# Performance work log

Hardware: AMD Instinct MI355X
Metric: run time of the kernel (lower is better)

## Reference

```python
import jax, jax.numpy as jnp
import numpy as np

B, D, H, S = 65536, 256, 4, 64
HD = D // H  # head_dim = 64
EPS = 1e-8


def _lin(x, W, b):
    # torch nn.Linear: y = x @ W.T + b, W: [out, in]
    return x @ W.T + b


def _cos_attn(q_heads, keys, vals):
    # q_heads: [B,H,hd]; keys/vals: [H,S,hd] (shared across batch)
    qn = q_heads / (jnp.linalg.norm(q_heads, axis=-1, keepdims=True) + EPS)
    kn = keys / (jnp.linalg.norm(keys, axis=-1, keepdims=True) + EPS)
    sim = jnp.einsum('bhd,hsd->bhs', qn, kn)          # cosine sims, temp=1.0
    attn = jax.nn.softmax(sim, axis=-1)
    return jnp.einsum('bhs,hsd->bhd', attn, vals)     # [B,H,hd]


def setup_inputs() -> dict:
    key = jax.random.key(0)
    ks = jax.random.split(key, 20)

    def xavier(k, shape):
        fan_in, fan_out = shape[1], shape[0]
        lim = np.sqrt(6.0 / (fan_in + fan_out))
        return jax.random.uniform(k, shape, jnp.float32, -lim, lim)

    return {
        'query': jax.random.normal(ks[0], (B, D), jnp.float32),
        'context': jax.random.normal(ks[1], (B, D), jnp.float32),
        'fast_keys': 0.01 * jax.random.normal(ks[2], (H, S, HD), jnp.float32),
        'fast_vals': 0.01 * jax.random.normal(ks[3], (H, S, HD), jnp.float32),
        'deep_keys': 0.01 * jax.random.normal(ks[4], (H, S, HD), jnp.float32),
        'deep_vals': 0.01 * jax.random.normal(ks[5], (H, S, HD), jnp.float32),
        'Wq': xavier(ks[6], (D, D)), 'bq': jnp.zeros((D,), jnp.float32),
        'Wg': xavier(ks[7], (D, D)), 'bg': jnp.zeros((D,), jnp.float32),
        'Wc1': xavier(ks[8], (D // 2, D)), 'bc1': jnp.zeros((D // 2,), jnp.float32),
        'Wc2': xavier(ks[9], (1, D // 2)), 'bc2': jnp.zeros((1,), jnp.float32),
        'Wo': xavier(ks[10], (D, D)), 'bo': jnp.zeros((D,), jnp.float32),
        'Ws': xavier(ks[11], (D, D)), 'bs': jnp.zeros((D,), jnp.float32),
        'mix_logit': jnp.zeros((), jnp.float32),
        'surprise_mean': jnp.zeros((1, D), jnp.float32),
        'surprise_var': jnp.ones((1, D), jnp.float32),
    }


def reference(query, context, fast_keys, fast_vals, deep_keys, deep_vals,
              Wq, bq, Wg, bg, Wc1, bc1, Wc2, bc2, Wo, bo, Ws, bs,
              mix_logit, surprise_mean, surprise_var):
    # --- query projection and head split ---
    q = _lin(query, Wq, bq)                       # [B, D]
    q_heads = q.reshape(B, H, HD)                 # [B, H, hd]

    # --- dual-tier cosine-similarity attention reads ---
    v_fast = _cos_attn(q_heads, fast_keys, fast_vals).reshape(B, D)
    v_deep = _cos_attn(q_heads, deep_keys, deep_vals).reshape(B, D)

    # --- context-gated mixing of tiers ---
    gate = jnp.tanh(_lin(context, Wg, bg)).mean(axis=-1, keepdims=True)  # [B,1]
    mix = jax.nn.sigmoid(mix_logit + gate)
    out = mix * v_fast + (1.0 - mix) * v_deep

    # --- adaptive retrieval confidence head ---
    conf = jax.nn.sigmoid(_lin(jnp.tanh(_lin(context, Wc1, bc1)), Wc2, bc2))  # [B,1]
    out = out * conf
    out = _lin(out, Wo, bo)                       # [B, d_value]

    # --- surprise (detached diagnostic, does not feed output) ---
    h = jax.lax.stop_gradient(_lin(context, Ws, bs))
    z = (h - surprise_mean) / jnp.sqrt(surprise_var + 1e-6)
    surprise = jax.nn.sigmoid(jnp.abs(z).mean(axis=-1) - 2.0)  # 1/max(0.5,0.1)=2.0
    del surprise  # aux diagnostic; main output is the retrieved vector
    return out
```

## Files before the change

kernel.cpp:

```cpp
#include <hip/hip_runtime.h>

typedef unsigned short u16;
typedef __attribute__((ext_vector_type(8))) short bf16x8;
typedef __attribute__((ext_vector_type(4))) float f32x4;
typedef __attribute__((ext_vector_type(8))) unsigned short u16x8;

#define MFMA16(a, b, c) __builtin_amdgcn_mfma_f32_16x16x32_bf16((a), (b), (c), 0, 0, 0)

#define OFF_WQ   0
#define OFF_WG   65536
#define OFF_WC1  131072
#define OFF_WO   163840
#define OFF_KNF  229376
#define OFF_VTF  245760
#define OFF_KND  262144
#define OFF_VTD  278528

__device__ __forceinline__ u16 f2b(float f) {
  union { float f; unsigned u; } v; v.f = f;
  unsigned r = v.u + 0x7fffu + ((v.u >> 16) & 1u);
  return (u16)(r >> 16);
}
__device__ __forceinline__ unsigned pk2(float lo, float hi) {
  unsigned r;
  asm("v_cvt_pk_bf16_f32 %0, %1, %2" : "=v"(r) : "v"(lo), "v"(hi));
  return r;
}
__device__ __forceinline__ float fsig(float x) {
  return __builtin_amdgcn_rcpf(1.f + __expf(-x));
}
__device__ __forceinline__ float ftanh(float x) {
  float e = __expf(2.f * x);
  return (e - 1.f) * __builtin_amdgcn_rcpf(e + 1.f);
}
__device__ __forceinline__ float sum16(float v) {
  v += __shfl_xor(v, 1);
  v += __shfl_xor(v, 2);
  v += __shfl_xor(v, 4);
  v += __shfl_xor(v, 8);
  return v;
}

__global__ void k_prep(const float* __restrict__ Wq, const float* __restrict__ Wg,
                       const float* __restrict__ Wc1, const float* __restrict__ Wo,
                       const float* __restrict__ fk, const float* __restrict__ fv,
                       const float* __restrict__ dk, const float* __restrict__ dv,
                       u16* __restrict__ ws) {
  const int bid = blockIdx.x, t = threadIdx.x;
  if (bid < 96) {
    const float* W = bid < 32 ? Wq : (bid < 64 ? Wg : Wo);
    const int OFF = bid < 32 ? OFF_WQ : (bid < 64 ? OFF_WG : OFF_WO);
    int c = (bid & 31) * 256 + t;
    int lane = c & 63, nt = (c >> 6) & 1, kk = (c >> 7) & 7, w = c >> 10;
    const float* s = W + (w * 32 + nt * 16 + (lane & 15)) * 256 + kk * 32 + ((lane >> 4) & 3) * 8;
    u16x8 o;
    #pragma unroll
    for (int j = 0; j < 8; ++j) o[j] = f2b(s[j]);
    *(u16x8*)(ws + OFF + c * 8) = o;
  } else if (bid < 112) {
    int c = (bid - 96) * 256 + t;
    int lane = c & 63, kk = (c >> 6) & 7, w = c >> 9;
    const float* s = Wc1 + (w * 16 + (lane & 15)) * 256 + kk * 32 + ((lane >> 4) & 3) * 8;
    u16x8 o;
    #pragma unroll
    for (int j = 0; j < 8; ++j) o[j] = f2b(s[j]);
    *(u16x8*)(ws + OFF_WC1 + c * 8) = o;
  } else {
    int unit = (bid - 112) * 4 + (t >> 6);
    int lane = t & 63;
    int st = unit >> 8, rowid = unit & 255;
    int hh = rowid >> 6, s = rowid & 63;
    if (st < 2) {
      const float* p = (st == 0 ? fk : dk) + rowid * 64;
      float x = p[lane];
      float v = x * x;
      v += __shfl_xor(v, 1);  v += __shfl_xor(v, 2);  v += __shfl_xor(v, 4);
      v += __shfl_xor(v, 8);  v += __shfl_xor(v, 16); v += __shfl_xor(v, 32);
      float sc = __builtin_amdgcn_rcpf(__builtin_amdgcn_sqrtf(v) + 1e-8f);
      int nt = s >> 4, kk = lane >> 5, lo = ((lane >> 3) & 3) * 16 + (s & 15), j = lane & 7;
      ws[(st == 0 ? OFF_KNF : OFF_KND) + (((hh * 2 + kk) * 4 + nt) * 64 + lo) * 8 + j] =
          f2b(x * sc);
    } else {
      const float* p = (st == 2 ? fv : dv) + rowid * 64;
      int kk = s >> 5, qd = (s >> 3) & 3, j = s & 7;
      int lo = qd * 16 + (lane & 15), nt = lane >> 4;
      ws[(st == 2 ? OFF_VTF : OFF_VTD) + (((hh * 2 + kk) * 4 + nt) * 64 + lo) * 8 + j] =
          f2b(p[lane]);
    }
  }
}

__global__ __launch_bounds__(512, 4)
void k_fused(const float* __restrict__ query, const float* __restrict__ context,
             const float* __restrict__ bq, const float* __restrict__ bg,
             const float* __restrict__ bc1, const float* __restrict__ Wc2,
             const float* __restrict__ bc2v, const float* __restrict__ bo,
             const float* __restrict__ mixl, const u16* __restrict__ ws,
             float* __restrict__ outp) {
  __shared__ u16 sX[64 * 256];
  __shared__ u16 sY[64 * 256];
  __shared__ float red_a[8][64];
  __shared__ float red_c[8][64];
  __shared__ float sA[64];
  __shared__ float sB[64];

  const int t = threadIdx.x;
  const int w = t >> 6;
  const int lane = t & 63;
  const int quad = lane >> 4;
  const int l16 = lane & 15;
  const int row4 = quad * 4;
  const int l16e = l16 & ~1;
  const int oddl = lane & 1;
  const int hd = w & 3;
  const int rb = (w >> 2) * 32;
  const int blk = blockIdx.x;
  char* Xb = (char*)sX;
  char* Yb = (char*)sY;
  char* Ch = Xb + w * 4096;

  auto stage = [&](char* dstB, const float* src) {
    #pragma unroll
    for (int i = 0; i < 8; ++i) {
      int e = i * 2048 + t * 4;
      float4 v = *(const float4*)(src + e);
      int row = e >> 8, col = e & 255;
      uint2 pk;
      pk.x = pk2(v.x, v.y);
      pk.y = pk2(v.z, v.w);
      *(uint2*)(dstB + row * 512 + ((((col >> 3) ^ (row & 7)) << 4) | ((col & 7) << 1))) = pk;
    }
  };
  auto ldA = [&](const char* B, int row, int kb) {
    return *(const bf16x8*)(B + row * 512 + ((((kb >> 3) ^ (row & 7)) << 4)));
  };
  auto ldCh = [&](int row, int kb) {
    return *(const bf16x8*)(Ch + row * 128 + ((((kb >> 3) ^ (row & 7)) << 4)));
  };
  auto st4c = [&](int row, float v0, float v1, float v2, float v3) {
    float o0 = __shfl_xor(v0, 1), o1 = __shfl_xor(v1, 1);
    float o2 = __shfl_xor(v2, 1), o3 = __shfl_xor(v3, 1);
    float lo0 = oddl ? o1 : v0, hi0 = oddl ? v1 : o0;
    float lo1 = oddl ? o3 : v2, hi1 = oddl ? v3 : o2;
    int c0 = (oddl ? 16 : 0) + l16e, c1 = (oddl ? 48 : 32) + l16e;
    *(unsigned*)(Ch + row * 128 + ((((c0 >> 3) ^ (row & 7)) << 4) | ((c0 & 7) << 1))) = pk2(lo0, hi0);
    *(unsigned*)(Ch + row * 128 + ((((c1 >> 3) ^ (row & 7)) << 4) | ((c1 & 7) << 1))) = pk2(lo1, hi1);
  };
  auto st4y = [&](int row, int cb, float v0, float v1, float v2, float v3) {
    float o0 = __shfl_xor(v0, 1), o1 = __shfl_xor(v1, 1);
    float o2 = __shfl_xor(v2, 1), o3 = __shfl_xor(v3, 1);
    float lo0 = oddl ? o1 : v0, hi0 = oddl ? v1 : o0;
    float lo1 = oddl ? o3 : v2, hi1 = oddl ? v3 : o2;
    int c0 = cb + (oddl ? 16 : 0) + l16e, c1 = cb + (oddl ? 48 : 32) + l16e;
    *(unsigned*)(Yb + row * 512 + ((((c0 >> 3) ^ (row & 7)) << 4) | ((c0 & 7) << 1))) = pk2(lo0, hi0);
    *(unsigned*)(Yb + row * 512 + ((((c1 >> 3) ^ (row & 7)) << 4) | ((c1 & 7) << 1))) = pk2(lo1, hi1);
  };

  const f32x4 vzero = {0.f, 0.f, 0.f, 0.f};

  bf16x8 pg0 = *(const bf16x8*)(ws + OFF_WG + ((w * 16 + 0) * 64 + lane) * 8);
  bf16x8 pg1 = *(const bf16x8*)(ws + OFF_WG + ((w * 16 + 1) * 64 + lane) * 8);
  bf16x8 pc0 = *(const bf16x8*)(ws + OFF_WC1 + ((w * 8) * 64 + lane) * 8);

  stage(Xb, context + (size_t)blk * 16384);
  stage(Yb, query + (size_t)blk * 16384);
  float bgv[2], bov[2], bq4[4];
  #pragma unroll
  for (int nt = 0; nt < 2; ++nt) {
    int n = w * 32 + nt * 16 + l16;
    bgv[nt] = bg[n]; bov[nt] = bo[n];
  }
  #pragma unroll
  for (int nt = 0; nt < 4; ++nt) bq4[nt] = bq[hd * 64 + nt * 16 + l16];
  float bc1v = bc1[w * 16 + l16];
  float wc2v = Wc2[w * 16 + l16];
  __syncthreads();

  bf16x8 pq0, pq1;
  {
    f32x4 ag[4][2], ac[4];
    #pragma unroll
    for (int mt = 0; mt < 4; ++mt) { ag[mt][0] = vzero; ag[mt][1] = vzero; ac[mt] = vzero; }
    #pragma unroll
    for (int kk = 0; kk < 8; ++kk) {
      int kb = kk * 32 + quad * 8;
      bf16x8 a0 = ldA(Xb, l16, kb), a1 = ldA(Xb, 16 + l16, kb),
             a2 = ldA(Xb, 32 + l16, kb), a3 = ldA(Xb, 48 + l16, kb);
      bf16x8 b0 = kk ? *(const bf16x8*)(ws + OFF_WG + (((w * 8 + kk) * 2 + 0) * 64 + lane) * 8) : pg0;
      bf16x8 b1 = kk ? *(const bf16x8*)(ws + OFF_WG + (((w * 8 + kk) * 2 + 1) * 64 + lane) * 8) : pg1;
      bf16x8 bc = kk ? *(const bf16x8*)(ws + OFF_WC1 + ((w * 8 + kk) * 64 + lane) * 8) : pc0;
      ag[0][0] = MFMA16(a0, b0, ag[0][0]); ag[0][1] = MFMA16(a0, b1, ag[0][1]);
      ag[1][0] = MFMA16(a1, b0, ag[1][0]); ag[1][1] = MFMA16(a1, b1, ag[1][1]);
      ag[2][0] = MFMA16(a2, b0, ag[2][0]); ag[2][1] = MFMA16(a2, b1, ag[2][1]);
      ag[3][0] = MFMA16(a3, b0, ag[3][0]); ag[3][1] = MFMA16(a3, b1, ag[3][1]);
      ac[0] = MFMA16(a0, bc, ac[0]);
      ac[1] = MFMA16(a1, bc, ac[1]);
      ac[2] = MFMA16(a2, bc, ac[2]);
      ac[3] = MFMA16(a3, bc, ac[3]);
    }
    pq0 = *(const bf16x8*)(ws + OFF_WQ + ((((hd * 4) >> 1) * 8 * 2 + ((hd * 4) & 1)) * 64 + lane) * 8);
    pq1 = *(const bf16x8*)(ws + OFF_WQ + (((((hd * 4 + 1) >> 1) * 8) * 2 + ((hd * 4 + 1) & 1)) * 64 + lane) * 8);
    #pragma unroll
    for (int mt = 0; mt < 4; ++mt)
      #pragma unroll
      for (int r = 0; r < 4; ++r) {
        float sg = ftanh(ag[mt][0][r] + bgv[0]) + ftanh(ag[mt][1][r] + bgv[1]);
        sg = sum16(sg);
        float sc = ftanh(ac[mt][r] + bc1v) * wc2v;
        sc = sum16(sc);
        if (l16 == 0) { red_a[w][mt * 16 + row4 + r] = sg; red_c[w][mt * 16 + row4 + r] = sc; }
      }
  }
  __syncthreads();

  if (t < 64) {
    float g = 0.f, cc = 0.f;
    #pragma unroll
    for (int i = 0; i < 8; ++i) { g += red_a[i][t]; cc += red_c[i][t]; }
    float mix = fsig(mixl[0] + g * (1.f / 256.f));
    float conf = fsig(cc + bc2v[0]);
    sA[t] = conf * mix;
    sB[t] = conf - conf * mix;
  }
  {
    f32x4 qa[2][4];
    #pragma unroll
    for (int mt = 0; mt < 2; ++mt)
      #pragma unroll
      for (int nt = 0; nt < 4; ++nt) qa[mt][nt] = vzero;
    #pragma unroll
    for (int kk = 0; kk < 8; ++kk) {
      int kb = kk * 32 + quad * 8;
      bf16x8 a0 = ldA(Yb, rb + l16, kb), a1 = ldA(Yb, rb + 16 + l16, kb);
      #pragma unroll
      for (int nt = 0; nt < 4; ++nt) {
        int g = hd * 4 + nt;
        bf16x8 b = (kk == 0 && nt == 0) ? pq0
                 : (kk == 0 && nt == 1) ? pq1
                 : *(const bf16x8*)(ws + OFF_WQ + ((((g >> 1) * 8 + kk) * 2 + (g & 1)) * 64 + lane) * 8);
        qa[0][nt] = MFMA16(a0, b, qa[0][nt]);
        qa[1][nt] = MFMA16(a1, b, qa[1][nt]);
      }
    }
    #pragma unroll
    for (int mt = 0; mt < 2; ++mt)
      #pragma unroll
      for (int r = 0; r < 4; ++r) {
        float ss = 0.f;
        #pragma unroll
        for (int nt = 0; nt < 4; ++nt) {
          float q_ = qa[mt][nt][r] + bq4[nt];
          qa[mt][nt][r] = q_;
          ss += q_ * q_;
        }
        ss = sum16(ss);
        float scl = __builtin_amdgcn_rcpf(__builtin_amdgcn_sqrtf(ss) + 1e-8f);
        st4c(mt * 16 + row4 + r,
             qa[mt][0][r] * scl, qa[mt][1][r] * scl, qa[mt][2][r] * scl, qa[mt][3][r] * scl);
      }
  }
  __syncthreads();

  #pragma unroll
  for (int half = 0; half < 2; ++half) {
    const int rl = half * 16;
    bf16x8 q0 = ldCh(rl + l16, quad * 8);
    bf16x8 q1 = ldCh(rl + l16, 32 + quad * 8);
    f32x4 oa[4];

    #pragma unroll
    for (int tier = 0; tier < 2; ++tier) {
      const u16* KN = ws + (tier == 0 ? OFF_KNF : OFF_KND);
      const u16* VT = ws + (tier == 0 ? OFF_VTF : OFF_VTD);

      f32x4 s4[4];
      #pragma unroll
      for (int nt = 0; nt < 4; ++nt) s4[nt] = vzero;
      #pragma unroll
      for (int kk = 0; kk < 2; ++kk)
        #pragma unroll
        for (int nt = 0; nt < 4; ++nt) {
          bf16x8 b = *(const bf16x8*)(KN + (((hd * 2 + kk) * 4 + nt) * 64 + lane) * 8);
          s4[nt] = MFMA16(kk ? q1 : q0, b, s4[nt]);
        }

      #pragma unroll
      for (int r = 0; r < 4; ++r) {
        float rs = 0.f;
        #pragma unroll
        for (int nt = 0; nt < 4; ++nt) { float e = __expf(s4[nt][r]); s4[nt][r] = e; rs += e; }
        rs = sum16(rs);
        float inv = __builtin_amdgcn_rcpf(rs);
        st4c(rl + row4 + r,
             s4[0][r] * inv, s4[1][r] * inv, s4[2][r] * inv, s4[3][r] * inv);
      }

      bf16x8 p0 = ldCh(rl + l16, quad * 8);
      bf16x8 p1 = ldCh(rl + l16, 32 + quad * 8);
      f32x4 pv4[4];
      #pragma unroll
      for (int nt = 0; nt < 4; ++nt) pv4[nt] = vzero;
      #pragma unroll
      for (int kk = 0; kk < 2; ++kk)
        #pragma unroll
        for (int nt = 0; nt < 4; ++nt) {
          bf16x8 b = *(const bf16x8*)(VT + (((hd * 2 + kk) * 4 + nt) * 64 + lane) * 8);
          pv4[nt] = MFMA16(kk ? p1 : p0, b, pv4[nt]);
        }

      #pragma unroll
      for (int r = 0; r < 4; ++r) {
        int rg = rb + rl + row4 + r;
        float m_ = (tier == 0) ? sA[rg] : sB[rg];
        #pragma unroll
        for (int nt = 0; nt < 4; ++nt) {
          if (tier == 0) oa[nt][r] = m_ * pv4[nt][r];
          else           oa[nt][r] += m_ * pv4[nt][r];
        }
      }
    }

    #pragma unroll
    for (int r = 0; r < 4; ++r)
      st4y(rb + rl + row4 + r, hd * 64, oa[0][r], oa[1][r], oa[2][r], oa[3][r]);
  }

  bf16x8 po0 = *(const bf16x8*)(ws + OFF_WO + (((w * 8) * 2 + 0) * 64 + lane) * 8);
  bf16x8 po1 = *(const bf16x8*)(ws + OFF_WO + (((w * 8) * 2 + 1) * 64 + lane) * 8);
  __syncthreads();

  {
    f32x4 o[4][2];
    #pragma unroll
    for (int mt = 0; mt < 4; ++mt) { o[mt][0] = vzero; o[mt][1] = vzero; }
    #pragma unroll
    for (int kk = 0; kk < 8; ++kk) {
      int kb = kk * 32 + quad * 8;
      bf16x8 a0 = ldA(Yb, l16, kb), a1 = ldA(Yb, 16 + l16, kb),
             a2 = ldA(Yb, 32 + l16, kb), a3 = ldA(Yb, 48 + l16, kb);
      #pragma unroll
      for (int nt = 0; nt < 2; ++nt) {
        bf16x8 b = (kk == 0 && nt == 0) ? po0
                 : (kk == 0 && nt == 1) ? po1
                 : *(const bf16x8*)(ws + OFF_WO + (((w * 8 + kk) * 2 + nt) * 64 + lane) * 8);
        o[0][nt] = MFMA16(a0, b, o[0][nt]);
        o[1][nt] = MFMA16(a1, b, o[1][nt]);
        o[2][nt] = MFMA16(a2, b, o[2][nt]);
        o[3][nt] = MFMA16(a3, b, o[3][nt]);
      }
    }
    float* dst = outp + (size_t)blk * 16384;
    #pragma unroll
    for (int mt = 0; mt < 4; ++mt)
      #pragma unroll
      for (int r = 0; r < 4; ++r) {
        int row = mt * 16 + row4 + r;
        #pragma unroll
        for (int nt = 0; nt < 2; ++nt)
          dst[row * 256 + w * 32 + nt * 16 + l16] = o[mt][nt][r] + bov[nt];
      }
  }
}

extern "C" void kernel_launch(void* const* d_in, const int* in_sizes, int n_in,
                              void* d_out, int out_size, void* d_ws, size_t ws_size,
                              hipStream_t stream) {
  const float* query   = (const float*)d_in[0];
  const float* context = (const float*)d_in[1];
  const float* fk      = (const float*)d_in[2];
  const float* fv      = (const float*)d_in[3];
  const float* dk      = (const float*)d_in[4];
  const float* dv      = (const float*)d_in[5];
  const float* Wq      = (const float*)d_in[6];
  const float* bq      = (const float*)d_in[7];
  const float* Wg      = (const float*)d_in[8];
  const float* bg      = (const float*)d_in[9];
  const float* Wc1     = (const float*)d_in[10];
  const float* bc1     = (const float*)d_in[11];
  const float* Wc2     = (const float*)d_in[12];
  const float* bc2     = (const float*)d_in[13];
  const float* Wo      = (const float*)d_in[14];
  const float* bo      = (const float*)d_in[15];
  const float* mixl    = (const float*)d_in[18];
  u16* ws = (u16*)d_ws;
  float* outp = (float*)d_out;

  k_prep<<<368, 256, 0, stream>>>(Wq, Wg, Wc1, Wo, fk, fv, dk, dv, ws);
  k_fused<<<1024, 512, 0, stream>>>(query, context, bq, bg, bc1, Wc2, bc2, bo,
                                    mixl, ws, outp);
}
```

Before: 276.3 us.

## Double block to 128 rows with 16 waves and dynamic shared memory

The fused kernel now processes 128 rows per block with 1024 threads (16 waves) instead of 64 rows with 512 threads. Each wave owns one 16-column weight fragment and sweeps all 8 row tiles, so each weight fragment is fetched once per 128 rows. Q-norm reduction now crosses waves through shared memory. It uses about 149 KB of dynamic LDS, limiting each CU to one block, which trades occupancy and latency hiding for weight reuse and fewer blocks.

```diff
diff --git a/kernel.cpp b/kernel.cpp
--- a/kernel.cpp
+++ b/kernel.cpp
@@ -90,19 +90,21 @@
   }
 }
 
-__global__ __launch_bounds__(512, 4)
+__global__ __launch_bounds__(1024, 4)
 void k_fused(const float* __restrict__ query, const float* __restrict__ context,
              const float* __restrict__ bq, const float* __restrict__ bg,
              const float* __restrict__ bc1, const float* __restrict__ Wc2,
              const float* __restrict__ bc2v, const float* __restrict__ bo,
              const float* __restrict__ mixl, const u16* __restrict__ ws,
              float* __restrict__ outp) {
-  __shared__ u16 sX[64 * 256];
-  __shared__ u16 sY[64 * 256];
-  __shared__ float red_a[8][64];
-  __shared__ float red_c[8][64];
-  __shared__ float sA[64];
-  __shared__ float sB[64];
+  extern __shared__ char smem[];
+  char* Xb = smem;
+  char* Yb = smem + 65536;
+  float* red_a = (float*)(smem + 131072);
+  float* red_c = (float*)(smem + 139264);
+  float* red_q = (float*)(smem + 143360);
+  float* sA    = (float*)(smem + 151552);
+  float* sB    = (float*)(smem + 152064);
 
   const int t = threadIdx.x;
   const int w = t >> 6;
@@ -114,15 +116,15 @@
   const int oddl = lane & 1;
   const int hd = w & 3;
   const int rb = (w >> 2) * 32;
+  const int hdc = w >> 2;
+  const int cg = w & 3;
   const int blk = blockIdx.x;
-  char* Xb = (char*)sX;
-  char* Yb = (char*)sY;
   char* Ch = Xb + w * 4096;
 
   auto stage = [&](char* dstB, const float* src) {
     #pragma unroll
     for (int i = 0; i < 8; ++i) {
-      int e = i * 2048 + t * 4;
+      int e = i * 4096 + t * 4;
       float4 v = *(const float4*)(src + e);
       int row = e >> 8, col = e & 255;
       uint2 pk;
@@ -136,6 +138,9 @@
   };
   auto ldCh = [&](int row, int kb) {
     return *(const bf16x8*)(Ch + row * 128 + ((((kb >> 3) ^ (row & 7)) << 4)));
+  };
+  auto wfrag = [&](int OFF, int g, int kk) {
+    return *(const bf16x8*)(ws + OFF + ((((g >> 1) * 8 + kk) * 2 + (g & 1)) * 64 + lane) * 8);
   };
   auto st4c = [&](int row, float v0, float v1, float v2, float v3) {
     float o0 = __shfl_xor(v0, 1), o1 = __shfl_xor(v1, 1);
@@ -158,207 +163,221 @@
 
   const f32x4 vzero = {0.f, 0.f, 0.f, 0.f};
 
-  bf16x8 pg0 = *(const bf16x8*)(ws + OFF_WG + ((w * 16 + 0) * 64 + lane) * 8);
-  bf16x8 pg1 = *(const bf16x8*)(ws + OFF_WG + ((w * 16 + 1) * 64 + lane) * 8);
-  bf16x8 pc0 = *(const bf16x8*)(ws + OFF_WC1 + ((w * 8) * 64 + lane) * 8);
-
-  stage(Xb, context + (size_t)blk * 16384);
-  stage(Yb, query + (size_t)blk * 16384);
-  float bgv[2], bov[2], bq4[4];
-  #pragma unroll
-  for (int nt = 0; nt < 2; ++nt) {
-    int n = w * 32 + nt * 16 + l16;
-    bgv[nt] = bg[n]; bov[nt] = bo[n];
-  }
-  #pragma unroll
-  for (int nt = 0; nt < 4; ++nt) bq4[nt] = bq[hd * 64 + nt * 16 + l16];
-  float bc1v = bc1[w * 16 + l16];
-  float wc2v = Wc2[w * 16 + l16];
+  stage(Xb, context + (size_t)blk * 32768);
+  stage(Yb, query + (size_t)blk * 32768);
+  float bgv  = bg[w * 16 + l16];
+  float bov  = bo[w * 16 + l16];
+  float bqv  = bq[w * 16 + l16];
+  float bc1v = bc1[(w & 7) * 16 + l16];
+  float wc2v = Wc2[(w & 7) * 16 + l16];
   __syncthreads();
 
-  bf16x8 pq0, pq1;
   {
-    f32x4 ag[4][2], ac[4];
-    #pragma unroll
-    for (int mt = 0; mt < 4; ++mt) { ag[mt][0] = vzero; ag[mt][1] = vzero; ac[mt] = vzero; }
+    f32x4 ag[8];
+    #pragma unroll
+    for (int mt = 0; mt < 8; ++mt) ag[mt] = vzero;
     #pragma unroll
     for (int kk = 0; kk < 8; ++kk) {
       int kb = kk * 32 + quad * 8;
-      bf16x8 a0 = ldA(Xb, l16, kb), a1 = ldA(Xb, 16 + l16, kb),
-             a2 = ldA(Xb, 32 + l16, kb), a3 = ldA(Xb, 48 + l16, kb);
-      bf16x8 b0 = kk ? *(const bf16x8*)(ws + OFF_WG + (((w * 8 + kk) * 2 + 0) * 64 + lane) * 8) : pg0;
-      bf16x8 b1 = kk ? *(const bf16x8*)(ws + OFF_WG + (((w * 8 + kk) * 2 + 1) * 64 + lane) * 8) : pg1;
-      bf16x8 bc = kk ? *(const bf16x8*)(ws + OFF_WC1 + ((w * 8 + kk) * 64 + lane) * 8) : pc0;
-      ag[0][0] = MFMA16(a0, b0, ag[0][0]); ag[0][1] = MFMA16(a0, b1, ag[0][1]);
-      ag[1][0] = MFMA16(a1, b0, ag[1][0]); ag[1][1] = MFMA16(a1, b1, ag[1][1]);
-      ag[2][0] = MFMA16(a2, b0, ag[2][0]); ag[2][1] = MFMA16(a2, b1, ag[2][1]);
-      ag[3][0] = MFMA16(a3, b0, ag[3][0]); ag[3][1] = MFMA16(a3, b1, ag[3][1]);
-      ac[0] = MFMA16(a0, bc, ac[0]);
-      ac[1] = MFMA16(a1, bc, ac[1]);
-      ac[2] = MFMA16(a2, bc, ac[2]);
-      ac[3] = MFMA16(a3, bc, ac[3]);
-    }
-    pq0 = *(const bf16x8*)(ws + OFF_WQ + ((((hd * 4) >> 1) * 8 * 2 + ((hd * 4) & 1)) * 64 + lane) * 8);
-    pq1 = *(const bf16x8*)(ws + OFF_WQ + (((((hd * 4 + 1) >> 1) * 8) * 2 + ((hd * 4 + 1) & 1)) * 64 + lane) * 8);
-    #pragma unroll
-    for (int mt = 0; mt < 4; ++mt)
+      bf16x8 b = wfrag(OFF_WG, w, kk);
+      #pragma unroll
+      for (int mt = 0; mt < 8; ++mt) {
+        bf16x8 a = ldA(Xb, mt * 16 + l16, kb);
+        ag[mt] = MFMA16(a, b, ag[mt]);
+      }
+    }
+    #pragma unroll
+    for (int mt = 0; mt < 8; ++mt)
       #pragma unroll
       for (int r = 0; r < 4; ++r) {
-        float sg = ftanh(ag[mt][0][r] + bgv[0]) + ftanh(ag[mt][1][r] + bgv[1]);
-        sg = sum16(sg);
-        float sc = ftanh(ac[mt][r] + bc1v) * wc2v;
-        sc = sum16(sc);
-        if (l16 == 0) { red_a[w][mt * 16 + row4 + r] = sg; red_c[w][mt * 16 + row4 + r] = sc; }
+        float sg = sum16(ftanh(ag[mt][r] + bgv));
+        if (l16 == 0) red_a[(mt * 16 + row4 + r) * 16 + w] = sg;
+      }
+  }
+  {
+    const int mtb = (w < 8) ? 0 : 4;
+    f32x4 ac[4];
+    #pragma unroll
+    for (int m = 0; m < 4; ++m) ac[m] = vzero;
+    #pragma unroll
+    for (int kk = 0; kk < 8; ++kk) {
+      int kb = kk * 32 + quad * 8;
+      bf16x8 b = *(const bf16x8*)(ws + OFF_WC1 + (((w & 7) * 8 + kk) * 64 + lane) * 8);
+      #pragma unroll
+      for (int m = 0; m < 4; ++m) {
+        bf16x8 a = ldA(Xb, (mtb + m) * 16 + l16, kb);
+        ac[m] = MFMA16(a, b, ac[m]);
+      }
+    }
+    #pragma unroll
+    for (int m = 0; m < 4; ++m)
+      #pragma unroll
+      for (int r = 0; r < 4; ++r) {
+        float sc = sum16(ftanh(ac[m][r] + bc1v) * wc2v);
+        if (l16 == 0) red_c[((mtb + m) * 16 + row4 + r) * 8 + (w & 7)] = sc;
       }
   }
   __syncthreads();
 
-  if (t < 64) {
+  if (t < 128) {
     float g = 0.f, cc = 0.f;
     #pragma unroll
-    for (int i = 0; i < 8; ++i) { g += red_a[i][t]; cc += red_c[i][t]; }
+    for (int i = 0; i < 4; ++i) {
+      f32x4 v = *(const f32x4*)(red_a + t * 16 + i * 4);
+      g += v[0] + v[1] + v[2] + v[3];
+    }
+    #pragma unroll
+    for (int i = 0; i < 2; ++i) {
+      f32x4 v = *(const f32x4*)(red_c + t * 8 + i * 4);
+      cc += v[0] + v[1] + v[2] + v[3];
+    }
     float mix = fsig(mixl[0] + g * (1.f / 256.f));
     float conf = fsig(cc + bc2v[0]);
     sA[t] = conf * mix;
     sB[t] = conf - conf * mix;
   }
+  f32x4 qa[8];
   {
-    f32x4 qa[2][4];
-    #pragma unroll
-    for (int mt = 0; mt < 2; ++mt)
-      #pragma unroll
-      for (int nt = 0; nt < 4; ++nt) qa[mt][nt] = vzero;
+    #pragma unroll
+    for (int mt = 0; mt < 8; ++mt) qa[mt] = vzero;
     #pragma unroll
     for (int kk = 0; kk < 8; ++kk) {
       int kb = kk * 32 + quad * 8;
-      bf16x8 a0 = ldA(Yb, rb + l16, kb), a1 = ldA(Yb, rb + 16 + l16, kb);
+      bf16x8 b = wfrag(OFF_WQ, w, kk);
+      #pragma unroll
+      for (int mt = 0; mt < 8; ++mt) {
+        bf16x8 a = ldA(Yb, mt * 16 + l16, kb);
+        qa[mt] = MFMA16(a, b, qa[mt]);
+      }
+    }
+    #pragma unroll
+    for (int mt = 0; mt < 8; ++mt)
+      #pragma unroll
+      for (int r = 0; r < 4; ++r) {
+        float q_ = qa[mt][r] + bqv;
+        qa[mt][r] = q_;
+        float ss = sum16(q_ * q_);
+        if (l16 == 0) red_q[(mt * 16 + row4 + r) * 16 + w] = ss;
+      }
+  }
+  __syncthreads();
+
+  #pragma unroll
+  for (int mt = 0; mt < 8; ++mt)
+    #pragma unroll
+    for (int r = 0; r < 4; ++r) {
+      int R = mt * 16 + row4 + r;
+      f32x4 p4 = *(const f32x4*)(red_q + R * 16 + hdc * 4);
+      float ss = p4[0] + p4[1] + p4[2] + p4[3];
+      float scl = __builtin_amdgcn_rcpf(__builtin_amdgcn_sqrtf(ss) + 1e-8f);
+      char* cb = Xb + (((R >> 5) * 4 + hdc) << 12);
+      int col = cg * 16 + l16, rr = R & 31;
+      *(u16*)(cb + rr * 128 + ((((col >> 3) ^ (rr & 7)) << 4) | ((col & 7) << 1))) =
+          f2b(qa[mt][r] * scl);
+    }
+  __syncthreads();
+
+  bf16x8 qf[2][2];
+  #pragma unroll
+  for (int h = 0; h < 2; ++h)
+    #pragma unroll
+    for (int kq = 0; kq < 2; ++kq)
+      qf[h][kq] = ldCh(h * 16 + l16, kq * 32 + quad * 8);
+
+  f32x4 oa[2][4];
+  #pragma unroll
+  for (int tier = 0; tier < 2; ++tier) {
+    const u16* KN = ws + (tier == 0 ? OFF_KNF : OFF_KND);
+    const u16* VT = ws + (tier == 0 ? OFF_VTF : OFF_VTD);
+
+    f32x4 s4[2][4];
+    #pragma unroll
+    for (int h = 0; h < 2; ++h)
+      #pragma unroll
+      for (int nt = 0; nt < 4; ++nt) s4[h][nt] = vzero;
+    #pragma unroll
+    for (int kk = 0; kk < 2; ++kk)
       #pragma unroll
       for (int nt = 0; nt < 4; ++nt) {
-        int g = hd * 4 + nt;
-        bf16x8 b = (kk == 0 && nt == 0) ? pq0
-                 : (kk == 0 && nt == 1) ? pq1
-                 : *(const bf16x8*)(ws + OFF_WQ + ((((g >> 1) * 8 + kk) * 2 + (g & 1)) * 64 + lane) * 8);
-        qa[0][nt] = MFMA16(a0, b, qa[0][nt]);
-        qa[1][nt] = MFMA16(a1, b, qa[1][nt]);
-      }
-    }
-    #pragma unroll
-    for (int mt = 0; mt < 2; ++mt)
-      #pragma unroll
-      for (int r = 0; r < 4; ++r) {
-        float ss = 0.f;
-        #pragma unroll
-        for (int nt = 0; nt < 4; ++nt) {
-          float q_ = qa[mt][nt][r] + bq4[nt];
-          qa[mt][nt][r] = q_;
-          ss += q_ * q_;
-        }
-        ss = sum16(ss);
-        float scl = __builtin_amdgcn_rcpf(__builtin_amdgcn_sqrtf(ss) + 1e-8f);
-        st4c(mt * 16 + row4 + r,
-             qa[mt][0][r] * scl, qa[mt][1][r] * scl, qa[mt][2][r] * scl, qa[mt][3][r] * scl);
-      }
-  }
-  __syncthreads();
-
-  #pragma unroll
-  for (int half = 0; half < 2; ++half) {
-    const int rl = half * 16;
-    bf16x8 q0 = ldCh(rl + l16, quad * 8);
-    bf16x8 q1 = ldCh(rl + l16, 32 + quad * 8);
-    f32x4 oa[4];
-
-    #pragma unroll
-    for (int tier = 0; tier < 2; ++tier) {
-      const u16* KN = ws + (tier == 0 ? OFF_KNF : OFF_KND);
-      const u16* VT = ws + (tier == 0 ? OFF_VTF : OFF_VTD);
-
-      f32x4 s4[4];
-      #pragma unroll
-      for (int nt = 0; nt < 4; ++nt) s4[nt] = vzero;
-      #pragma unroll
-      for (int kk = 0; kk < 2; ++kk)
-        #pragma unroll
-        for (int nt = 0; nt < 4; ++nt) {
-          bf16x8 b = *(const bf16x8*)(KN + (((hd * 2 + kk) * 4 + nt) * 64 + lane) * 8);
-          s4[nt] = MFMA16(kk ? q1 : q0, b, s4[nt]);
-        }
-
+        bf16x8 b = *(const bf16x8*)(KN + (((hd * 2 + kk) * 4 + nt) * 64 + lane) * 8);
+        s4[0][nt] = MFMA16(qf[0][kk], b, s4[0][nt]);
+        s4[1][nt] = MFMA16(qf[1][kk], b, s4[1][nt]);
+      }
+
+    #pragma unroll
+    for (int h = 0; h < 2; ++h)
       #pragma unroll
       for (int r = 0; r < 4; ++r) {
         float rs = 0.f;
         #pragma unroll
-        for (int nt = 0; nt < 4; ++nt) { float e = __expf(s4[nt][r]); s4[nt][r] = e; rs += e; }
+        for (int nt = 0; nt < 4; ++nt) { float e = __expf(s4[h][nt][r]); s4[h][nt][r] = e; rs += e; }
         rs = sum16(rs);
         float inv = __builtin_amdgcn_rcpf(rs);
-        st4c(rl + row4 + r,
-             s4[0][r] * inv, s4[1][r] * inv, s4[2][r] * inv, s4[3][r] * inv);
-      }
-
-      bf16x8 p0 = ldCh(rl + l16, quad * 8);
-      bf16x8 p1 = ldCh(rl + l16, 32 + quad * 8);
-      f32x4 pv4[4];
-      #pragma unroll
-      for (int nt = 0; nt < 4; ++nt) pv4[nt] = vzero;
-      #pragma unroll
-      for (int kk = 0; kk < 2; ++kk)
+        st4c(h * 16 + row4 + r,
+             s4[h][0][r] * inv, s4[h][1][r] * inv, s4[h][2][r] * inv, s4[h][3][r] * inv);
+      }
+
+    bf16x8 pf[2][2];
+    #pragma unroll
+    for (int h = 0; h < 2; ++h) {
+      pf[h][0] = ldCh(h * 16 + l16, quad * 8);
+      pf[h][1] = ldCh(h * 16 + l16, 32 + quad * 8);
+    }
+    f32x4 pv[2][4];
+    #pragma unroll
+    for (int h = 0; h < 2; ++h)
+      #pragma unroll
+      for (int nt = 0; nt < 4; ++nt) pv[h][nt] = vzero;
+    #pragma unroll
+    for (int kk = 0; kk < 2; ++kk)
+      #pragma unroll
+      for (int nt = 0; nt < 4; ++nt) {
+        bf16x8 b = *(const bf16x8*)(VT + (((hd * 2 + kk) * 4 + nt) * 64 + lane) * 8);
+        pv[0][nt] = MFMA16(pf[0][kk], b, pv[0][nt]);
+        pv[1][nt] = MFMA16(pf[1][kk], b, pv[1][nt]);
+      }
+
+    #pragma unroll
+    for (int h = 0; h < 2; ++h)
+      #pragma unroll
+      for (int r = 0; r < 4; ++r) {
+        int Rb = rb + h * 16 + row4 + r;
+        float m_ = (tier == 0) ? sA[Rb] : sB[Rb];
         #pragma unroll
         for (int nt = 0; nt < 4; ++nt) {
-          bf16x8 b = *(const bf16x8*)(VT + (((hd * 2 + kk) * 4 + nt) * 64 + lane) * 8);
-          pv4[nt] = MFMA16(kk ? p1 : p0, b, pv4[nt]);
+          if (tier == 0) oa[h][nt][r] = m_ * pv[h][nt][r];
+          else           oa[h][nt][r] += m_ * pv[h][nt][r];
         }
-
-      #pragma unroll
-      for (int r = 0; r < 4; ++r) {
-        int rg = rb + rl + row4 + r;
-        float m_ = (tier == 0) ? sA[rg] : sB[rg];
-        #pragma unroll
-        for (int nt = 0; nt < 4; ++nt) {
-          if (tier == 0) oa[nt][r] = m_ * pv4[nt][r];
-          else           oa[nt][r] += m_ * pv4[nt][r];
-        }
-      }
-    }
-
+      }
+  }
+
+  #pragma unroll
+  for (int h = 0; h < 2; ++h)
     #pragma unroll
     for (int r = 0; r < 4; ++r)
-      st4y(rb + rl + row4 + r, hd * 64, oa[0][r], oa[1][r], oa[2][r], oa[3][r]);
-  }
-
-  bf16x8 po0 = *(const bf16x8*)(ws + OFF_WO + (((w * 8) * 2 + 0) * 64 + lane) * 8);
-  bf16x8 po1 = *(const bf16x8*)(ws + OFF_WO + (((w * 8) * 2 + 1) * 64 + lane) * 8);
+      st4y(rb + h * 16 + row4 + r, hd * 64, oa[h][0][r], oa[h][1][r], oa[h][2][r], oa[h][3][r]);
   __syncthreads();
 
   {
-    f32x4 o[4][2];
-    #pragma unroll
-    for (int mt = 0; mt < 4; ++mt) { o[mt][0] = vzero; o[mt][1] = vzero; }
+    f32x4 o[8];
+    #pragma unroll
+    for (int mt = 0; mt < 8; ++mt) o[mt] = vzero;
     #pragma unroll
     for (int kk = 0; kk < 8; ++kk) {
       int kb = kk * 32 + quad * 8;
-      bf16x8 a0 = ldA(Yb, l16, kb), a1 = ldA(Yb, 16 + l16, kb),
-             a2 = ldA(Yb, 32 + l16, kb), a3 = ldA(Yb, 48 + l16, kb);
-      #pragma unroll
-      for (int nt = 0; nt < 2; ++nt) {
-        bf16x8 b = (kk == 0 && nt == 0) ? po0
-                 : (kk == 0 && nt == 1) ? po1
-                 : *(const bf16x8*)(ws + OFF_WO + (((w * 8 + kk) * 2 + nt) * 64 + lane) * 8);
-        o[0][nt] = MFMA16(a0, b, o[0][nt]);
-        o[1][nt] = MFMA16(a1, b, o[1][nt]);
-        o[2][nt] = MFMA16(a2, b, o[2][nt]);
-        o[3][nt] = MFMA16(a3, b, o[3][nt]);
-      }
-    }
-    float* dst = outp + (size_t)blk * 16384;
-    #pragma unroll
-    for (int mt = 0; mt < 4; ++mt)
-      #pragma unroll
-      for (int r = 0; r < 4; ++r) {
-        int row = mt * 16 + row4 + r;
-        #pragma unroll
-        for (int nt = 0; nt < 2; ++nt)
-          dst[row * 256 + w * 32 + nt * 16 + l16] = o[mt][nt][r] + bov[nt];
-      }
+      bf16x8 b = wfrag(OFF_WO, w, kk);
+      #pragma unroll
+      for (int mt = 0; mt < 8; ++mt) {
+        bf16x8 a = ldA(Yb, mt * 16 + l16, kb);
+        o[mt] = MFMA16(a, b, o[mt]);
+      }
+    }
+    float* dst = outp + (size_t)blk * 32768;
+    #pragma unroll
+    for (int mt = 0; mt < 8; ++mt)
+      #pragma unroll
+      for (int r = 0; r < 4; ++r)
+        dst[(mt * 16 + row4 + r) * 256 + w * 16 + l16] = o[mt][r] + bov;
   }
 }
 
@@ -386,6 +405,6 @@
   float* outp = (float*)d_out;
 
   k_prep<<<368, 256, 0, stream>>>(Wq, Wg, Wc1, Wo, fk, fv, dk, dv, ws);
-  k_fused<<<1024, 512, 0, stream>>>(query, context, bq, bg, bc1, Wc2, bc2, bo,
-                                    mixl, ws, outp);
-}
+  k_fused<<<512, 1024, 152576, stream>>>(query, context, bq, bg, bc1, Wc2, bc2, bo,
+                                         mixl, ws, outp);
+}
```

New measurement: 313.1 us. 1.13x slower.

## Reuse one shared tile for context and query to raise occupancy

Applied to the files above, without the earlier changes.

Replaces the separate context and query shared tiles with one 32 KB buffer. Query is loaded into registers during the gate/confidence epilogue and written into the same buffer after a barrier. The per-wave scratch is halved by keeping the second half of the normalized queries in registers until the first half is consumed. Launch bounds are raised to 6 blocks per CU so more workgroups fit in LDS. The cost is an extra barrier and more live registers (qv, qa held across phases), which could cause spills under the tighter register budget.

```diff
diff --git a/kernel.cpp b/kernel.cpp
--- a/kernel.cpp
+++ b/kernel.cpp
@@ -90,19 +90,20 @@
   }
 }
 
-__global__ __launch_bounds__(512, 4)
+__global__ __launch_bounds__(512, 6)
 void k_fused(const float* __restrict__ query, const float* __restrict__ context,
              const float* __restrict__ bq, const float* __restrict__ bg,
              const float* __restrict__ bc1, const float* __restrict__ Wc2,
              const float* __restrict__ bc2v, const float* __restrict__ bo,
              const float* __restrict__ mixl, const u16* __restrict__ ws,
              float* __restrict__ outp) {
-  __shared__ u16 sX[64 * 256];
-  __shared__ u16 sY[64 * 256];
-  __shared__ float red_a[8][64];
-  __shared__ float red_c[8][64];
-  __shared__ float sA[64];
-  __shared__ float sB[64];
+  extern __shared__ char smem[];
+  char* Mb = smem;
+  char* Cb = smem + 32768;
+  float (*red_a)[64] = (float(*)[64])(smem + 49152);
+  float (*red_c)[64] = (float(*)[64])(smem + 51200);
+  float* sA = (float*)(smem + 53248);
+  float* sB = (float*)(smem + 53504);
 
   const int t = threadIdx.x;
   const int w = t >> 6;
@@ -115,24 +116,10 @@
   const int hd = w & 3;
   const int rb = (w >> 2) * 32;
   const int blk = blockIdx.x;
-  char* Xb = (char*)sX;
-  char* Yb = (char*)sY;
-  char* Ch = Xb + w * 4096;
-
-  auto stage = [&](char* dstB, const float* src) {
-    #pragma unroll
-    for (int i = 0; i < 8; ++i) {
-      int e = i * 2048 + t * 4;
-      float4 v = *(const float4*)(src + e);
-      int row = e >> 8, col = e & 255;
-      uint2 pk;
-      pk.x = pk2(v.x, v.y);
-      pk.y = pk2(v.z, v.w);
-      *(uint2*)(dstB + row * 512 + ((((col >> 3) ^ (row & 7)) << 4) | ((col & 7) << 1))) = pk;
-    }
-  };
-  auto ldA = [&](const char* B, int row, int kb) {
-    return *(const bf16x8*)(B + row * 512 + ((((kb >> 3) ^ (row & 7)) << 4)));
+  char* Ch = Cb + w * 2048;
+
+  auto ldA = [&](int row, int kb) {
+    return *(const bf16x8*)(Mb + row * 512 + ((((kb >> 3) ^ (row & 7)) << 4)));
   };
   auto ldCh = [&](int row, int kb) {
     return *(const bf16x8*)(Ch + row * 128 + ((((kb >> 3) ^ (row & 7)) << 4)));
@@ -146,14 +133,14 @@
     *(unsigned*)(Ch + row * 128 + ((((c0 >> 3) ^ (row & 7)) << 4) | ((c0 & 7) << 1))) = pk2(lo0, hi0);
     *(unsigned*)(Ch + row * 128 + ((((c1 >> 3) ^ (row & 7)) << 4) | ((c1 & 7) << 1))) = pk2(lo1, hi1);
   };
-  auto st4y = [&](int row, int cb, float v0, float v1, float v2, float v3) {
+  auto st4m = [&](int row, int cb, float v0, float v1, float v2, float v3) {
     float o0 = __shfl_xor(v0, 1), o1 = __shfl_xor(v1, 1);
     float o2 = __shfl_xor(v2, 1), o3 = __shfl_xor(v3, 1);
     float lo0 = oddl ? o1 : v0, hi0 = oddl ? v1 : o0;
     float lo1 = oddl ? o3 : v2, hi1 = oddl ? v3 : o2;
     int c0 = cb + (oddl ? 16 : 0) + l16e, c1 = cb + (oddl ? 48 : 32) + l16e;
-    *(unsigned*)(Yb + row * 512 + ((((c0 >> 3) ^ (row & 7)) << 4) | ((c0 & 7) << 1))) = pk2(lo0, hi0);
-    *(unsigned*)(Yb + row * 512 + ((((c1 >> 3) ^ (row & 7)) << 4) | ((c1 & 7) << 1))) = pk2(lo1, hi1);
+    *(unsigned*)(Mb + row * 512 + ((((c0 >> 3) ^ (row & 7)) << 4) | ((c0 & 7) << 1))) = pk2(lo0, hi0);
+    *(unsigned*)(Mb + row * 512 + ((((c1 >> 3) ^ (row & 7)) << 4) | ((c1 & 7) << 1))) = pk2(lo1, hi1);
   };
 
   const f32x4 vzero = {0.f, 0.f, 0.f, 0.f};
@@ -161,9 +148,19 @@
   bf16x8 pg0 = *(const bf16x8*)(ws + OFF_WG + ((w * 16 + 0) * 64 + lane) * 8);
   bf16x8 pg1 = *(const bf16x8*)(ws + OFF_WG + ((w * 16 + 1) * 64 + lane) * 8);
   bf16x8 pc0 = *(const bf16x8*)(ws + OFF_WC1 + ((w * 8) * 64 + lane) * 8);
-
-  stage(Xb, context + (size_t)blk * 16384);
-  stage(Yb, query + (size_t)blk * 16384);
+  {
+    const float* src = context + (size_t)blk * 16384;
+    #pragma unroll
+    for (int i = 0; i < 8; ++i) {
+      int e = i * 2048 + t * 4;
+      float4 v = *(const float4*)(src + e);
+      int row = e >> 8, col = e & 255;
+      uint2 pk;
+      pk.x = pk2(v.x, v.y);
+      pk.y = pk2(v.z, v.w);
+      *(uint2*)(Mb + row * 512 + ((((col >> 3) ^ (row & 7)) << 4) | ((col & 7) << 1))) = pk;
+    }
+  }
   float bgv[2], bov[2], bq4[4];
   #pragma unroll
   for (int nt = 0; nt < 2; ++nt) {
@@ -176,7 +173,7 @@
   float wc2v = Wc2[w * 16 + l16];
   __syncthreads();
 
-  bf16x8 pq0, pq1;
+  float4 qv[8];
   {
     f32x4 ag[4][2], ac[4];
     #pragma unroll
@@ -184,8 +181,8 @@
     #pragma unroll
     for (int kk = 0; kk < 8; ++kk) {
       int kb = kk * 32 + quad * 8;
-      bf16x8 a0 = ldA(Xb, l16, kb), a1 = ldA(Xb, 16 + l16, kb),
-             a2 = ldA(Xb, 32 + l16, kb), a3 = ldA(Xb, 48 + l16, kb);
+      bf16x8 a0 = ldA(l16, kb), a1 = ldA(16 + l16, kb),
+             a2 = ldA(32 + l16, kb), a3 = ldA(48 + l16, kb);
       bf16x8 b0 = kk ? *(const bf16x8*)(ws + OFF_WG + (((w * 8 + kk) * 2 + 0) * 64 + lane) * 8) : pg0;
       bf16x8 b1 = kk ? *(const bf16x8*)(ws + OFF_WG + (((w * 8 + kk) * 2 + 1) * 64 + lane) * 8) : pg1;
       bf16x8 bc = kk ? *(const bf16x8*)(ws + OFF_WC1 + ((w * 8 + kk) * 64 + lane) * 8) : pc0;
@@ -198,21 +195,39 @@
       ac[2] = MFMA16(a2, bc, ac[2]);
       ac[3] = MFMA16(a3, bc, ac[3]);
     }
-    pq0 = *(const bf16x8*)(ws + OFF_WQ + ((((hd * 4) >> 1) * 8 * 2 + ((hd * 4) & 1)) * 64 + lane) * 8);
-    pq1 = *(const bf16x8*)(ws + OFF_WQ + (((((hd * 4 + 1) >> 1) * 8) * 2 + ((hd * 4 + 1) & 1)) * 64 + lane) * 8);
     #pragma unroll
     for (int mt = 0; mt < 4; ++mt)
       #pragma unroll
       for (int r = 0; r < 4; ++r) {
         float sg = ftanh(ag[mt][0][r] + bgv[0]) + ftanh(ag[mt][1][r] + bgv[1]);
         sg = sum16(sg);
+        if (l16 == 0) red_a[w][mt * 16 + row4 + r] = sg;
+      }
+    {
+      const float* qsrc = query + (size_t)blk * 16384;
+      #pragma unroll
+      for (int i = 0; i < 8; ++i) qv[i] = *(const float4*)(qsrc + i * 2048 + t * 4);
+    }
+    #pragma unroll
+    for (int mt = 0; mt < 4; ++mt)
+      #pragma unroll
+      for (int r = 0; r < 4; ++r) {
         float sc = ftanh(ac[mt][r] + bc1v) * wc2v;
         sc = sum16(sc);
-        if (l16 == 0) { red_a[w][mt * 16 + row4 + r] = sg; red_c[w][mt * 16 + row4 + r] = sc; }
+        if (l16 == 0) red_c[w][mt * 16 + row4 + r] = sc;
       }
   }
   __syncthreads();
 
+  #pragma unroll
+  for (int i = 0; i < 8; ++i) {
+    int e = i * 2048 + t * 4;
+    int row = e >> 8, col = e & 255;
+    uint2 pk;
+    pk.x = pk2(qv[i].x, qv[i].y);
+    pk.y = pk2(qv[i].z, qv[i].w);
+    *(uint2*)(Mb + row * 512 + ((((col >> 3) ^ (row & 7)) << 4) | ((col & 7) << 1))) = pk;
+  }
   if (t < 64) {
     float g = 0.f, cc = 0.f;
     #pragma unroll
@@ -222,8 +237,16 @@
     sA[t] = conf * mix;
     sB[t] = conf - conf * mix;
   }
+  bf16x8 pq[4];
+  #pragma unroll
+  for (int nt = 0; nt < 4; ++nt) {
+    int g = hd * 4 + nt;
+    pq[nt] = *(const bf16x8*)(ws + OFF_WQ + ((((g >> 1) * 8) * 2 + (g & 1)) * 64 + lane) * 8);
+  }
+  __syncthreads();
+
+  f32x4 qa[2][4];
   {
-    f32x4 qa[2][4];
     #pragma unroll
     for (int mt = 0; mt < 2; ++mt)
       #pragma unroll
@@ -231,13 +254,12 @@
     #pragma unroll
     for (int kk = 0; kk < 8; ++kk) {
       int kb = kk * 32 + quad * 8;
-      bf16x8 a0 = ldA(Yb, rb + l16, kb), a1 = ldA(Yb, rb + 16 + l16, kb);
+      bf16x8 a0 = ldA(rb + l16, kb), a1 = ldA(rb + 16 + l16, kb);
       #pragma unroll
       for (int nt = 0; nt < 4; ++nt) {
         int g = hd * 4 + nt;
-        bf16x8 b = (kk == 0 && nt == 0) ? pq0
-                 : (kk == 0 && nt == 1) ? pq1
-                 : *(const bf16x8*)(ws + OFF_WQ + ((((g >> 1) * 8 + kk) * 2 + (g & 1)) * 64 + lane) * 8);
+        bf16x8 b = kk ? *(const bf16x8*)(ws + OFF_WQ + ((((g >> 1) * 8 + kk) * 2 + (g & 1)) * 64 + lane) * 8)
+                      : pq[nt];
         qa[0][nt] = MFMA16(a0, b, qa[0][nt]);
         qa[1][nt] = MFMA16(a1, b, qa[1][nt]);
       }
@@ -255,17 +277,19 @@
         }
         ss = sum16(ss);
         float scl = __builtin_amdgcn_rcpf(__builtin_amdgcn_sqrtf(ss) + 1e-8f);
-        st4c(mt * 16 + row4 + r,
-             qa[mt][0][r] * scl, qa[mt][1][r] * scl, qa[mt][2][r] * scl, qa[mt][3][r] * scl);
-      }
+        #pragma unroll
+        for (int nt = 0; nt < 4; ++nt) qa[mt][nt][r] *= scl;
+      }
+    #pragma unroll
+    for (int r = 0; r < 4; ++r)
+      st4c(row4 + r, qa[0][0][r], qa[0][1][r], qa[0][2][r], qa[0][3][r]);
   }
   __syncthreads();
 
   #pragma unroll
   for (int half = 0; half < 2; ++half) {
-    const int rl = half * 16;
-    bf16x8 q0 = ldCh(rl + l16, quad * 8);
-    bf16x8 q1 = ldCh(rl + l16, 32 + quad * 8);
+    bf16x8 q0 = ldCh(l16, quad * 8);
+    bf16x8 q1 = ldCh(l16, 32 + quad * 8);
     f32x4 oa[4];
 
     #pragma unroll
@@ -291,12 +315,11 @@
         for (int nt = 0; nt < 4; ++nt) { float e = __expf(s4[nt][r]); s4[nt][r] = e; rs += e; }
         rs = sum16(rs);
         float inv = __builtin_amdgcn_rcpf(rs);
-        st4c(rl + row4 + r,
-             s4[0][r] * inv, s4[1][r] * inv, s4[2][r] * inv, s4[3][r] * inv);
-      }
-
-      bf16x8 p0 = ldCh(rl + l16, quad * 8);
-      bf16x8 p1 = ldCh(rl + l16, 32 + quad * 8);
+        st4c(row4 + r, s4[0][r] * inv, s4[1][r] * inv, s4[2][r] * inv, s4[3][r] * inv);
+      }
+
+      bf16x8 p0 = ldCh(l16, quad * 8);
+      bf16x8 p1 = ldCh(l16, 32 + quad * 8);
       f32x4 pv4[4];
       #pragma unroll
       for (int nt = 0; nt < 4; ++nt) pv4[nt] = vzero;
@@ -310,8 +333,8 @@
 
       #pragma unroll
       for (int r = 0; r < 4; ++r) {
-        int rg = rb + rl + row4 + r;
-        float m_ = (tier == 0) ? sA[rg] : sB[rg];
+        int Rg = rb + half * 16 + row4 + r;
+        float m_ = (tier == 0) ? sA[Rg] : sB[Rg];
         #pragma unroll
         for (int nt = 0; nt < 4; ++nt) {
           if (tier == 0) oa[nt][r] = m_ * pv4[nt][r];
@@ -320,9 +343,14 @@
       }
     }
 
+    if (half == 0) {
+      #pragma unroll
+      for (int r = 0; r < 4; ++r)
+        st4c(row4 + r, qa[1][0][r], qa[1][1][r], qa[1][2][r], qa[1][3][r]);
+    }
     #pragma unroll
     for (int r = 0; r < 4; ++r)
-      st4y(rb + rl + row4 + r, hd * 64, oa[0][r], oa[1][r], oa[2][r], oa[3][r]);
+      st4m(rb + half * 16 + row4 + r, hd * 64, oa[0][r], oa[1][r], oa[2][r], oa[3][r]);
   }
 
   bf16x8 po0 = *(const bf16x8*)(ws + OFF_WO + (((w * 8) * 2 + 0) * 64 + lane) * 8);
@@ -336,8 +364,8 @@
     #pragma unroll
     for (int kk = 0; kk < 8; ++kk) {
       int kb = kk * 32 + quad * 8;
-      bf16x8 a0 = ldA(Yb, l16, kb), a1 = ldA(Yb, 16 + l16, kb),
-             a2 = ldA(Yb, 32 + l16, kb), a3 = ldA(Yb, 48 + l16, kb);
+      bf16x8 a0 = ldA(l16, kb), a1 = ldA(16 + l16, kb),
+             a2 = ldA(32 + l16, kb), a3 = ldA(48 + l16, kb);
       #pragma unroll
       for (int nt = 0; nt < 2; ++nt) {
         bf16x8 b = (kk == 0 && nt == 0) ? po0
@@ -386,6 +414,6 @@
   float* outp = (float*)d_out;
 
   k_prep<<<368, 256, 0, stream>>>(Wq, Wg, Wc1, Wo, fk, fv, dk, dv, ws);
-  k_fused<<<1024, 512, 0, stream>>>(query, context, bq, bg, bc1, Wc2, bc2, bo,
-                                    mixl, ws, outp);
-}
+  k_fused<<<1024, 512, 53760, stream>>>(query, context, bq, bg, bc1, Wc2, bc2, bo,
+                                        mixl, ws, outp);
+}
```

Result: slower. 343.1 us (+24.2%).
